# Optimization experiments

Measured on AMD Instinct MI355X. Metric: run time of the kernel, lower is better.

The kernel has to match this reference:

```python
import jax, jax.numpy as jnp
import numpy as np

N_HEADS = 16

def setup_inputs() -> dict:
    key = jax.random.key(0)
    qkv = jax.random.normal(key, (4, 3072, 1024), dtype=jnp.float32)
    return {"qkv": qkv}

def reference(qkv):
    bs, width, length = qkv.shape
    ch = width // (3 * N_HEADS)
    qkv_h = qkv.reshape(bs * N_HEADS, 3 * ch, length)
    q, k, v = jnp.split(qkv_h, 3, axis=1)  # each [bs*H, ch, T]
    scale = 1.0 / jnp.sqrt(jnp.sqrt(jnp.asarray(ch, qkv.dtype)))
    # [bs*H, T, T] scores
    weight = jnp.einsum('bct,bcs->bts', q * scale, k * scale)
    weight = jax.nn.softmax(weight.astype(jnp.float32), axis=-1).astype(weight.dtype)
    a = jnp.einsum('bts,bcs->bct', weight, v)  # [bs*H, ch, T]
    return a.reshape(bs, -1, length)
```

## Files before the change

### kernel.cpp

```cpp
#include <hip/hip_runtime.h>
#include <hip/hip_bf16.h>


typedef __bf16 bf16_8 __attribute__((ext_vector_type(8)));
typedef __bf16 bf16_4 __attribute__((ext_vector_type(4)));
typedef float floatx4 __attribute__((ext_vector_type(4)));

#define NTHREADS 256
#define STR 64
#define NSTEPS 16

#if __has_builtin(__builtin_amdgcn_exp2f)
#define EXP2(x) __builtin_amdgcn_exp2f(x)
#else
#define EXP2(x) exp2f(x)
#endif
#define QSCALE 0.18033688011112042f

#define LDS_BYTES 57344

__device__ __forceinline__ int kap(int row) { return ((row >> 1) + (row >> 4)) & 7; }

__global__ __launch_bounds__(NTHREADS, 2)
void attn_kernel(const float* __restrict__ qkv, float* __restrict__ out) {
    __shared__ char smem[LDS_BYTES];
    __bf16* q_s = (__bf16*)smem;
    __bf16* k0  = (__bf16*)(smem + 16384);
    __bf16* k1  = (__bf16*)(smem + 24576);
    __bf16* v0  = (__bf16*)(smem + 32768);
    __bf16* v1  = (__bf16*)(smem + 40960);
    __bf16* v2  = (__bf16*)(smem + 49152);

    const int tid  = threadIdx.x;
    const int wave = tid >> 6;
    const int lane = tid & 63;
    const int quad = lane >> 4;
    const int i16  = lane & 15;

    const int bx = blockIdx.x;
    const int bh = bx & 63;
    const int t0 = (bx >> 6) << 7;

    const float* qg = qkv + (size_t)bh * 196608;
    const float* kg = qg + 65536;
    const float* vg = qg + 131072;

    const int si = tid & 15;
    const int sG = tid >> 4;
    const int c0 = sG << 2;

    #pragma unroll
    for (int j = 0; j < 2; ++j) {
        int f  = j * NTHREADS + tid;
        int cG = f >> 5;
        int ti = f & 31;
        float4 q4[4];
        #pragma unroll
        for (int jj = 0; jj < 4; ++jj)
            q4[jj] = *(const float4*)(qg + (cG * 4 + jj) * 1024 + t0 + ti * 4);
        #pragma unroll
        for (int rr = 0; rr < 4; ++rr) {
            int trow = ti * 4 + rr;
            bf16_4 w;
            w[0] = (__bf16)(((const float*)&q4[0])[rr] * QSCALE);
            w[1] = (__bf16)(((const float*)&q4[1])[rr] * QSCALE);
            w[2] = (__bf16)(((const float*)&q4[2])[rr] * QSCALE);
            w[3] = (__bf16)(((const float*)&q4[3])[rr] * QSCALE);
            *(bf16_4*)&q_s[trow * STR + ((cG ^ (kap(trow) << 1)) << 2)] = w;
        }
    }
    {
        float4 k4[4], v4[4];
        #pragma unroll
        for (int jj = 0; jj < 4; ++jj) {
            k4[jj] = *(const float4*)(kg + (c0 + jj) * 1024 + si * 4);
            v4[jj] = *(const float4*)(vg + (c0 + jj) * 1024 + si * 4);
        }
        #pragma unroll
        for (int rr = 0; rr < 4; ++rr) {
            int srow = si * 4 + rr;
            bf16_4 w;
            w[0] = (__bf16)((const float*)&k4[0])[rr];
            w[1] = (__bf16)((const float*)&k4[1])[rr];
            w[2] = (__bf16)((const float*)&k4[2])[rr];
            w[3] = (__bf16)((const float*)&k4[3])[rr];
            *(bf16_4*)&k0[srow * STR + ((sG ^ (kap(srow) << 1)) << 2)] = w;
        }
        #pragma unroll
        for (int jj = 0; jj < 4; ++jj) {
            int c = c0 + jj;
            bf16_4 w;
            w[0] = (__bf16)v4[jj].x; w[1] = (__bf16)v4[jj].y;
            w[2] = (__bf16)v4[jj].z; w[3] = (__bf16)v4[jj].w;
            *(bf16_4*)&v0[c * STR + ((si ^ (kap(c) << 1)) << 2)] = w;
        }
    }
    __syncthreads();

    bf16_8 qf[2][2];
    #pragma unroll
    for (int tt = 0; tt < 2; ++tt) {
        int row = wave * 32 + tt * 16 + i16;
        int x = kap(row);
        #pragma unroll
        for (int kk = 0; kk < 2; ++kk)
            qf[tt][kk] = *(const bf16_8*)&q_s[row * STR + ((((kk << 2) | quad) ^ x) << 3)];
    }

    floatx4 O[2][4];
    #pragma unroll
    for (int tt = 0; tt < 2; ++tt)
        #pragma unroll
        for (int cn = 0; cn < 4; ++cn) O[tt][cn] = (floatx4){0.f, 0.f, 0.f, 0.f};
    float l[2] = {0.f, 0.f};

    __bf16* pw = q_s + (size_t)(wave * 32) * STR;
    const int xp0 = (i16 >> 1) & 7;

    bf16_8 afp[2][2];
    int vprev = 2, vcur = 0, vnext = 1;

    for (int is = 0; is < NSTEPS; ++is) {
        const __bf16* kc = (is & 1) ? k1 : k0;

        float4 kr[4], vr[4];
        if (is < NSTEPS - 1) {
            const int s0n = (is + 1) * 64;
            #pragma unroll
            for (int jj = 0; jj < 4; ++jj) {
                kr[jj] = *(const float4*)(kg + (c0 + jj) * 1024 + s0n + si * 4);
                vr[jj] = *(const float4*)(vg + (c0 + jj) * 1024 + s0n + si * 4);
            }
        }

        floatx4 St[2][4];
        #pragma unroll
        for (int sb = 0; sb < 4; ++sb) {
            int srow = sb * 16 + i16;
            int x = (sb + (i16 >> 1)) & 7;
            bf16_8 kf0 = *(const bf16_8*)&kc[srow * STR + ((quad ^ x) << 3)];
            bf16_8 kf1 = *(const bf16_8*)&kc[srow * STR + (((4 | quad) ^ x) << 3)];
            floatx4 a0 = (floatx4){0.f, 0.f, 0.f, 0.f};
            floatx4 a1 = (floatx4){0.f, 0.f, 0.f, 0.f};
            a0 = __builtin_amdgcn_mfma_f32_16x16x32_bf16(kf0, qf[0][0], a0, 0, 0, 0);
            a0 = __builtin_amdgcn_mfma_f32_16x16x32_bf16(kf1, qf[0][1], a0, 0, 0, 0);
            a1 = __builtin_amdgcn_mfma_f32_16x16x32_bf16(kf0, qf[1][0], a1, 0, 0, 0);
            a1 = __builtin_amdgcn_mfma_f32_16x16x32_bf16(kf1, qf[1][1], a1, 0, 0, 0);
            St[0][sb] = a0;
            St[1][sb] = a1;
        }
        #pragma unroll
        for (int tt = 0; tt < 2; ++tt) {
            int trow = tt * 16 + i16;
            int xp = (tt + xp0) & 7;
            #pragma unroll
            for (int sb = 0; sb < 4; ++sb) {
                float p0 = EXP2(St[tt][sb][0]);
                float p1 = EXP2(St[tt][sb][1]);
                float p2 = EXP2(St[tt][sb][2]);
                float p3 = EXP2(St[tt][sb][3]);
                l[tt] += (p0 + p1) + (p2 + p3);
                bf16_4 pk;
                pk[0] = (__bf16)p0; pk[1] = (__bf16)p1;
                pk[2] = (__bf16)p2; pk[3] = (__bf16)p3;
                int ch = ((sb << 2) | quad) ^ (xp << 1);
                *(bf16_4*)&pw[trow * STR + (ch << 2)] = pk;
            }
        }
        bf16_8 af[2][2];
        #pragma unroll
        for (int tt = 0; tt < 2; ++tt) {
            int trow = tt * 16 + i16;
            int xp = (tt + xp0) & 7;
            #pragma unroll
            for (int kk = 0; kk < 2; ++kk)
                af[tt][kk] = *(const bf16_8*)&pw[trow * STR + ((((kk << 2) | quad) ^ xp) << 3)];
        }

        if (is > 0) {
            const __bf16* vp = (vprev == 0) ? v0 : ((vprev == 1) ? v1 : v2);
            #pragma unroll
            for (int cn = 0; cn < 4; ++cn) {
                int crow = cn * 16 + i16;
                int xc = (cn + (i16 >> 1)) & 7;
                #pragma unroll
                for (int kk = 0; kk < 2; ++kk) {
                    bf16_8 vf = *(const bf16_8*)&vp[crow * STR + ((((kk << 2) | quad) ^ xc) << 3)];
                    O[0][cn] = __builtin_amdgcn_mfma_f32_16x16x32_bf16(vf, afp[0][kk], O[0][cn], 0, 0, 0);
                    O[1][cn] = __builtin_amdgcn_mfma_f32_16x16x32_bf16(vf, afp[1][kk], O[1][cn], 0, 0, 0);
                }
            }
        }
        #pragma unroll
        for (int tt = 0; tt < 2; ++tt)
            #pragma unroll
            for (int kk = 0; kk < 2; ++kk)
                afp[tt][kk] = af[tt][kk];

        if (is < NSTEPS - 1) {
            __bf16* kn = (is & 1) ? k0 : k1;
            __bf16* vn = (vnext == 0) ? v0 : ((vnext == 1) ? v1 : v2);
            #pragma unroll
            for (int rr = 0; rr < 4; ++rr) {
                int srow = si * 4 + rr;
                bf16_4 w;
                w[0] = (__bf16)((const float*)&kr[0])[rr];
                w[1] = (__bf16)((const float*)&kr[1])[rr];
                w[2] = (__bf16)((const float*)&kr[2])[rr];
                w[3] = (__bf16)((const float*)&kr[3])[rr];
                *(bf16_4*)&kn[srow * STR + ((sG ^ (kap(srow) << 1)) << 2)] = w;
            }
            #pragma unroll
            for (int jj = 0; jj < 4; ++jj) {
                int c = c0 + jj;
                bf16_4 w;
                w[0] = (__bf16)vr[jj].x; w[1] = (__bf16)vr[jj].y;
                w[2] = (__bf16)vr[jj].z; w[3] = (__bf16)vr[jj].w;
                *(bf16_4*)&vn[c * STR + ((si ^ (kap(c) << 1)) << 2)] = w;
            }
            __syncthreads();
        }
        vprev = vcur; vcur = vnext; vnext = (vnext == 2) ? 0 : vnext + 1;
    }

    {
        const __bf16* vp = (vprev == 0) ? v0 : ((vprev == 1) ? v1 : v2);
        #pragma unroll
        for (int cn = 0; cn < 4; ++cn) {
            int crow = cn * 16 + i16;
            int xc = (cn + (i16 >> 1)) & 7;
            #pragma unroll
            for (int kk = 0; kk < 2; ++kk) {
                bf16_8 vf = *(const bf16_8*)&vp[crow * STR + ((((kk << 2) | quad) ^ xc) << 3)];
                O[0][cn] = __builtin_amdgcn_mfma_f32_16x16x32_bf16(vf, afp[0][kk], O[0][cn], 0, 0, 0);
                O[1][cn] = __builtin_amdgcn_mfma_f32_16x16x32_bf16(vf, afp[1][kk], O[1][cn], 0, 0, 0);
            }
        }
    }

    float* og = out + (size_t)bh * 65536 + t0 + wave * 32;
    #pragma unroll
    for (int tt = 0; tt < 2; ++tt) {
        float s = l[tt];
        s += __shfl_xor(s, 16);
        s += __shfl_xor(s, 32);
        const float linv = 1.0f / s;
        #pragma unroll
        for (int cn = 0; cn < 4; ++cn)
            #pragma unroll
            for (int r = 0; r < 4; ++r)
                og[(cn * 16 + 4 * quad + r) * 1024 + tt * 16 + i16] = O[tt][cn][r] * linv;
    }
}

extern "C" void kernel_launch(void* const* d_in, const int* in_sizes, int n_in,
                              void* d_out, int out_size, void* d_ws, size_t ws_size,
                              hipStream_t stream) {
    const float* qkv = (const float*)d_in[0];
    float* out = (float*)d_out;
    attn_kernel<<<dim3(512), dim3(NTHREADS), 0, stream>>>(qkv, out);
}
```

Baseline: 106.0 us.

## Use 8 waves of 16 query rows and transpose P in registers via permlane swaps

```diff
diff --git a/kernel.cpp b/kernel.cpp
--- a/kernel.cpp
+++ b/kernel.cpp
@@ -6,7 +6,7 @@
 typedef __bf16 bf16_4 __attribute__((ext_vector_type(4)));
 typedef float floatx4 __attribute__((ext_vector_type(4)));
 
-#define NTHREADS 256
+#define NTHREADS 512
 #define STR 64
 #define NSTEPS 16
 
@@ -21,7 +21,42 @@
 
 __device__ __forceinline__ int kap(int row) { return ((row >> 1) + (row >> 4)) & 7; }
 
-__global__ __launch_bounds__(NTHREADS, 2)
+__device__ __forceinline__ unsigned pk_bf16(float a, float b) {
+    unsigned r;
+    asm("v_cvt_pk_bf16_f32 %0, %1, %2" : "=v"(r) : "v"(a), "v"(b));
+    return r;
+}
+__device__ __forceinline__ void swap32(unsigned& x, unsigned& y) {
+    asm("v_permlane32_swap_b32 %0, %1" : "+v"(x), "+v"(y));
+}
+__device__ __forceinline__ void swap16(unsigned& x, unsigned& y) {
+    asm("v_permlane16_swap_b32 %0, %1" : "+v"(x), "+v"(y));
+}
+
+__device__ __forceinline__ void write_k(__bf16* kn, const float4* r, int si, int sG) {
+    #pragma unroll
+    for (int rr = 0; rr < 4; ++rr) {
+        int srow = si * 4 + rr;
+        bf16_4 w;
+        w[0] = (__bf16)((const float*)&r[0])[rr];
+        w[1] = (__bf16)((const float*)&r[1])[rr];
+        w[2] = (__bf16)((const float*)&r[2])[rr];
+        w[3] = (__bf16)((const float*)&r[3])[rr];
+        *(bf16_4*)&kn[srow * STR + ((sG ^ (kap(srow) << 1)) << 2)] = w;
+    }
+}
+__device__ __forceinline__ void write_v(__bf16* vn, const float4* r, int si, int c0) {
+    #pragma unroll
+    for (int jj = 0; jj < 4; ++jj) {
+        int c = c0 + jj;
+        bf16_4 w;
+        w[0] = (__bf16)r[jj].x; w[1] = (__bf16)r[jj].y;
+        w[2] = (__bf16)r[jj].z; w[3] = (__bf16)r[jj].w;
+        *(bf16_4*)&vn[c * STR + ((si ^ (kap(c) << 1)) << 2)] = w;
+    }
+}
+
+__global__ __launch_bounds__(NTHREADS, 4)
 void attn_kernel(const float* __restrict__ qkv, float* __restrict__ out) {
     __shared__ char smem[LDS_BYTES];
     __bf16* q_s = (__bf16*)smem;
@@ -45,15 +80,16 @@
     const float* kg = qg + 65536;
     const float* vg = qg + 131072;
 
-    const int si = tid & 15;
-    const int sG = tid >> 4;
+    const int sv = tid >> 8;
+    const int st = tid & 255;
+    const int si = st & 15;
+    const int sG = st >> 4;
     const int c0 = sG << 2;
-
-    #pragma unroll
-    for (int j = 0; j < 2; ++j) {
-        int f  = j * NTHREADS + tid;
-        int cG = f >> 5;
-        int ti = f & 31;
+    const float* gsrc = sv ? vg : kg;
+
+    {
+        const int cG = tid >> 5;
+        const int ti = tid & 31;
         float4 q4[4];
         #pragma unroll
         for (int jj = 0; jj < 4; ++jj)
@@ -70,111 +106,77 @@
         }
     }
     {
-        float4 k4[4], v4[4];
-        #pragma unroll
-        for (int jj = 0; jj < 4; ++jj) {
-            k4[jj] = *(const float4*)(kg + (c0 + jj) * 1024 + si * 4);
-            v4[jj] = *(const float4*)(vg + (c0 + jj) * 1024 + si * 4);
-        }
-        #pragma unroll
-        for (int rr = 0; rr < 4; ++rr) {
-            int srow = si * 4 + rr;
-            bf16_4 w;
-            w[0] = (__bf16)((const float*)&k4[0])[rr];
-            w[1] = (__bf16)((const float*)&k4[1])[rr];
-            w[2] = (__bf16)((const float*)&k4[2])[rr];
-            w[3] = (__bf16)((const float*)&k4[3])[rr];
-            *(bf16_4*)&k0[srow * STR + ((sG ^ (kap(srow) << 1)) << 2)] = w;
-        }
-        #pragma unroll
-        for (int jj = 0; jj < 4; ++jj) {
-            int c = c0 + jj;
-            bf16_4 w;
-            w[0] = (__bf16)v4[jj].x; w[1] = (__bf16)v4[jj].y;
-            w[2] = (__bf16)v4[jj].z; w[3] = (__bf16)v4[jj].w;
-            *(bf16_4*)&v0[c * STR + ((si ^ (kap(c) << 1)) << 2)] = w;
-        }
+        float4 r4[4];
+        #pragma unroll
+        for (int jj = 0; jj < 4; ++jj)
+            r4[jj] = *(const float4*)(gsrc + (c0 + jj) * 1024 + si * 4);
+        if (!sv) write_k(k0, r4, si, sG);
+        else     write_v(v0, r4, si, c0);
     }
     __syncthreads();
 
-    bf16_8 qf[2][2];
-    #pragma unroll
-    for (int tt = 0; tt < 2; ++tt) {
-        int row = wave * 32 + tt * 16 + i16;
+    bf16_8 qf[2];
+    {
+        int row = wave * 16 + i16;
         int x = kap(row);
         #pragma unroll
         for (int kk = 0; kk < 2; ++kk)
-            qf[tt][kk] = *(const bf16_8*)&q_s[row * STR + ((((kk << 2) | quad) ^ x) << 3)];
-    }
-
-    floatx4 O[2][4];
-    #pragma unroll
-    for (int tt = 0; tt < 2; ++tt)
-        #pragma unroll
-        for (int cn = 0; cn < 4; ++cn) O[tt][cn] = (floatx4){0.f, 0.f, 0.f, 0.f};
-    float l[2] = {0.f, 0.f};
-
-    __bf16* pw = q_s + (size_t)(wave * 32) * STR;
-    const int xp0 = (i16 >> 1) & 7;
-
-    bf16_8 afp[2][2];
+            qf[kk] = *(const bf16_8*)&q_s[row * STR + ((((kk << 2) | quad) ^ x) << 3)];
+    }
+
+    floatx4 O[4];
+    #pragma unroll
+    for (int cn = 0; cn < 4; ++cn) O[cn] = (floatx4){0.f, 0.f, 0.f, 0.f};
+    float l = 0.f;
+
+    bf16_8 afp[2];
     int vprev = 2, vcur = 0, vnext = 1;
 
     for (int is = 0; is < NSTEPS; ++is) {
         const __bf16* kc = (is & 1) ? k1 : k0;
 
-        float4 kr[4], vr[4];
+        float4 pr[4];
         if (is < NSTEPS - 1) {
             const int s0n = (is + 1) * 64;
             #pragma unroll
-            for (int jj = 0; jj < 4; ++jj) {
-                kr[jj] = *(const float4*)(kg + (c0 + jj) * 1024 + s0n + si * 4);
-                vr[jj] = *(const float4*)(vg + (c0 + jj) * 1024 + s0n + si * 4);
-            }
-        }
-
-        floatx4 St[2][4];
+            for (int jj = 0; jj < 4; ++jj)
+                pr[jj] = *(const float4*)(gsrc + (c0 + jj) * 1024 + s0n + si * 4);
+        }
+
+        floatx4 St[4];
         #pragma unroll
         for (int sb = 0; sb < 4; ++sb) {
             int srow = sb * 16 + i16;
             int x = (sb + (i16 >> 1)) & 7;
             bf16_8 kf0 = *(const bf16_8*)&kc[srow * STR + ((quad ^ x) << 3)];
             bf16_8 kf1 = *(const bf16_8*)&kc[srow * STR + (((4 | quad) ^ x) << 3)];
-            floatx4 a0 = (floatx4){0.f, 0.f, 0.f, 0.f};
-            floatx4 a1 = (floatx4){0.f, 0.f, 0.f, 0.f};
-            a0 = __builtin_amdgcn_mfma_f32_16x16x32_bf16(kf0, qf[0][0], a0, 0, 0, 0);
-            a0 = __builtin_amdgcn_mfma_f32_16x16x32_bf16(kf1, qf[0][1], a0, 0, 0, 0);
-            a1 = __builtin_amdgcn_mfma_f32_16x16x32_bf16(kf0, qf[1][0], a1, 0, 0, 0);
-            a1 = __builtin_amdgcn_mfma_f32_16x16x32_bf16(kf1, qf[1][1], a1, 0, 0, 0);
-            St[0][sb] = a0;
-            St[1][sb] = a1;
-        }
-        #pragma unroll
-        for (int tt = 0; tt < 2; ++tt) {
-            int trow = tt * 16 + i16;
-            int xp = (tt + xp0) & 7;
-            #pragma unroll
-            for (int sb = 0; sb < 4; ++sb) {
-                float p0 = EXP2(St[tt][sb][0]);
-                float p1 = EXP2(St[tt][sb][1]);
-                float p2 = EXP2(St[tt][sb][2]);
-                float p3 = EXP2(St[tt][sb][3]);
-                l[tt] += (p0 + p1) + (p2 + p3);
-                bf16_4 pk;
-                pk[0] = (__bf16)p0; pk[1] = (__bf16)p1;
-                pk[2] = (__bf16)p2; pk[3] = (__bf16)p3;
-                int ch = ((sb << 2) | quad) ^ (xp << 1);
-                *(bf16_4*)&pw[trow * STR + (ch << 2)] = pk;
-            }
-        }
-        bf16_8 af[2][2];
-        #pragma unroll
-        for (int tt = 0; tt < 2; ++tt) {
-            int trow = tt * 16 + i16;
-            int xp = (tt + xp0) & 7;
-            #pragma unroll
-            for (int kk = 0; kk < 2; ++kk)
-                af[tt][kk] = *(const bf16_8*)&pw[trow * STR + ((((kk << 2) | quad) ^ xp) << 3)];
+            floatx4 a = (floatx4){0.f, 0.f, 0.f, 0.f};
+            a = __builtin_amdgcn_mfma_f32_16x16x32_bf16(kf0, qf[0], a, 0, 0, 0);
+            a = __builtin_amdgcn_mfma_f32_16x16x32_bf16(kf1, qf[1], a, 0, 0, 0);
+            St[sb] = a;
+        }
+
+        unsigned c01[4], c23[4];
+        #pragma unroll
+        for (int sb = 0; sb < 4; ++sb) {
+            float p0 = EXP2(St[sb][0]);
+            float p1 = EXP2(St[sb][1]);
+            float p2 = EXP2(St[sb][2]);
+            float p3 = EXP2(St[sb][3]);
+            l += (p0 + p1) + (p2 + p3);
+            c01[sb] = pk_bf16(p0, p1);
+            c23[sb] = pk_bf16(p2, p3);
+        }
+        bf16_8 af[2];
+        #pragma unroll
+        for (int kk = 0; kk < 2; ++kk) {
+            unsigned x0 = c01[2 * kk], y0 = c01[2 * kk + 1];
+            unsigned x1 = c23[2 * kk], y1 = c23[2 * kk + 1];
+            swap32(x0, y0); swap16(x0, y0);
+            swap32(x1, y1); swap16(x1, y1);
+            union { unsigned u[4]; bf16_8 v; } t;
+            t.u[0] = x0; t.u[1] = x1; t.u[2] = y0; t.u[3] = y1;
+            af[kk] = t.v;
         }
 
         if (is > 0) {
@@ -186,37 +188,19 @@
                 #pragma unroll
                 for (int kk = 0; kk < 2; ++kk) {
                     bf16_8 vf = *(const bf16_8*)&vp[crow * STR + ((((kk << 2) | quad) ^ xc) << 3)];
-                    O[0][cn] = __builtin_amdgcn_mfma_f32_16x16x32_bf16(vf, afp[0][kk], O[0][cn], 0, 0, 0);
-                    O[1][cn] = __builtin_amdgcn_mfma_f32_16x16x32_bf16(vf, afp[1][kk], O[1][cn], 0, 0, 0);
+                    O[cn] = __builtin_amdgcn_mfma_f32_16x16x32_bf16(vf, afp[kk], O[cn], 0, 0, 0);
                 }
             }
         }
-        #pragma unroll
-        for (int tt = 0; tt < 2; ++tt)
-            #pragma unroll
-            for (int kk = 0; kk < 2; ++kk)
-                afp[tt][kk] = af[tt][kk];
+        afp[0] = af[0]; afp[1] = af[1];
 
         if (is < NSTEPS - 1) {
-            __bf16* kn = (is & 1) ? k0 : k1;
-            __bf16* vn = (vnext == 0) ? v0 : ((vnext == 1) ? v1 : v2);
-            #pragma unroll
-            for (int rr = 0; rr < 4; ++rr) {
-                int srow = si * 4 + rr;
-                bf16_4 w;
-                w[0] = (__bf16)((const float*)&kr[0])[rr];
-                w[1] = (__bf16)((const float*)&kr[1])[rr];
-                w[2] = (__bf16)((const float*)&kr[2])[rr];
-                w[3] = (__bf16)((const float*)&kr[3])[rr];
-                *(bf16_4*)&kn[srow * STR + ((sG ^ (kap(srow) << 1)) << 2)] = w;
-            }
-            #pragma unroll
-            for (int jj = 0; jj < 4; ++jj) {
-                int c = c0 + jj;
-                bf16_4 w;
-                w[0] = (__bf16)vr[jj].x; w[1] = (__bf16)vr[jj].y;
-                w[2] = (__bf16)vr[jj].z; w[3] = (__bf16)vr[jj].w;
-                *(bf16_4*)&vn[c * STR + ((si ^ (kap(c) << 1)) << 2)] = w;
+            if (!sv) {
+                __bf16* kn = (is & 1) ? k0 : k1;
+                write_k(kn, pr, si, sG);
+            } else {
+                __bf16* vn = (vnext == 0) ? v0 : ((vnext == 1) ? v1 : v2);
+                write_v(vn, pr, si, c0);
             }
             __syncthreads();
         }
@@ -232,25 +216,21 @@
             #pragma unroll
             for (int kk = 0; kk < 2; ++kk) {
                 bf16_8 vf = *(const bf16_8*)&vp[crow * STR + ((((kk << 2) | quad) ^ xc) << 3)];
-                O[0][cn] = __builtin_amdgcn_mfma_f32_16x16x32_bf16(vf, afp[0][kk], O[0][cn], 0, 0, 0);
-                O[1][cn] = __builtin_amdgcn_mfma_f32_16x16x32_bf16(vf, afp[1][kk], O[1][cn], 0, 0, 0);
+                O[cn] = __builtin_amdgcn_mfma_f32_16x16x32_bf16(vf, afp[kk], O[cn], 0, 0, 0);
             }
         }
     }
 
-    float* og = out + (size_t)bh * 65536 + t0 + wave * 32;
-    #pragma unroll
-    for (int tt = 0; tt < 2; ++tt) {
-        float s = l[tt];
-        s += __shfl_xor(s, 16);
-        s += __shfl_xor(s, 32);
-        const float linv = 1.0f / s;
-        #pragma unroll
-        for (int cn = 0; cn < 4; ++cn)
-            #pragma unroll
-            for (int r = 0; r < 4; ++r)
-                og[(cn * 16 + 4 * quad + r) * 1024 + tt * 16 + i16] = O[tt][cn][r] * linv;
-    }
+    float s = l;
+    s += __shfl_xor(s, 16);
+    s += __shfl_xor(s, 32);
+    const float linv = 1.0f / s;
+    float* og = out + (size_t)bh * 65536 + t0 + wave * 16;
+    #pragma unroll
+    for (int cn = 0; cn < 4; ++cn)
+        #pragma unroll
+        for (int r = 0; r < 4; ++r)
+            og[(cn * 16 + 4 * quad + r) * 1024 + i16] = O[cn][r] * linv;
 }
 
 extern "C" void kernel_launch(void* const* d_in, const int* in_sizes, int n_in,
```

Measured after the change: 103.1 us. 2.7% less time.
